# Performance work log

Measured on AMD Instinct MI355X. Metric: run time of the kernel, lower is better.

Reference implementation:

```python
import jax, jax.numpy as jnp
import numpy as np

K = 7  # kernel_size


def setup_inputs() -> dict:
    key = jax.random.key(0)
    k1, k2 = jax.random.split(key)
    kernels = jax.random.normal(k1, (4, K, K, 256, 256), dtype=jnp.float32)
    features = jax.random.normal(k2, (4, 96, 256, 256), dtype=jnp.float32)
    return {"kernels": kernels, "features": features}


def reference(kernels, features):
    # kernels: [b, k, k, h, w]; features: [b, c, h, w]
    # Equivalent to unfold(features) viewed as [b,c,k,k,h,w] contracted with
    # kernels via einsum 'bcklhw,bklhw->bchw', but computed as a fused sum of
    # k*k shifted products to avoid materializing the k^2-larger intermediate.
    b, c, h, w = features.shape
    k = kernels.shape[1]
    p = k // 2
    fpad = jnp.pad(features, ((0, 0), (0, 0), (p, p), (p, p)))
    out = jnp.zeros_like(features)
    for i in range(k):  # small fixed loop over kernel taps (k*k = 49)
        for j in range(k):
            out = out + fpad[:, :, i:i + h, j:j + w] * kernels[:, i, j][:, None]
    return out
```

## Files before the change

### kernel.cpp

```cpp
#include <hip/hip_runtime.h>
#include <hip/hip_bf16.h>


#define BATCH 4
#define CHAN 96
#define HW_ 256
#define HWPIX 65536
#define KS 7
#define XT 64
#define YT 16
#define NTHR 512
#define BT_K 24
#define BT_NROW (KS * BT_K)
#define BT_STRIP (16 * BT_NROW + 8)
#define BT_BUF (4 * BT_STRIP)
#define KVALS (KS * KS * XT)
#define KSPT 7
#define FTOT ((size_t)BATCH * CHAN * HWPIX)

typedef __attribute__((ext_vector_type(8))) short short8v;
typedef __attribute__((ext_vector_type(4))) float f32x4;

union S8 { short8v s; unsigned u[4]; };

static __device__ __forceinline__ unsigned pkbf(float a, float b) {
    union { __hip_bfloat162 h; unsigned u; } c;
    c.h = __float22bfloat162_rn(make_float2(a, b));
    return c.u;
}
static __device__ __forceinline__ short bfbits(float x) {
    union { __hip_bfloat16 h; short s; } c;
    c.h = __float2bfloat16(x);
    return c.s;
}

struct AF { float4 v[3][2]; };

__global__ __launch_bounds__(NTHR)
void svconv_mfma4(const float* __restrict__ K_, const float* __restrict__ F_,
                  float* __restrict__ O_) {
    __shared__ short BT[2 * BT_BUF];

    const int tid = threadIdx.x;
    const int xt = blockIdx.x, yt = blockIdx.y, b = blockIdx.z;
    const int gx0 = xt * XT, gy0 = yt * YT;
    const int wave = tid >> 6, lane = tid & 63;
    const int nt = wave & 3, ch = wave >> 2;
    const int n = lane & 15, kb = lane >> 4;

    const int xs = gx0 - 4 + nt * 16 + kb * 8;
    const float* lo = F_;
    const float* hiq = F_ + FTOT - 4;
    const float* abase[3];
#pragma unroll
    for (int ct = 0; ct < 3; ++ct)
        abase[ct] = F_ + ((size_t)(b * CHAN + ch * 48 + ct * 16 + n)) * HWPIX + xs;

    unsigned xm[4];
#pragma unroll
    for (int i = 0; i < 4; ++i) {
        unsigned m0 = ((unsigned)(xs + 2 * i) < (unsigned)HW_) ? 0xFFFFu : 0u;
        unsigned m1 = ((unsigned)(xs + 2 * i + 1) < (unsigned)HW_) ? 0xFFFFu : 0u;
        xm[i] = m0 | (m1 << 16);
    }

    short8v ar[8][3];

    auto issueA = [&](int yr, AF& f) {
#pragma unroll
        for (int ct = 0; ct < 3; ++ct) {
            const float* p = abase[ct] + (size_t)yr * HW_;
            const float* p0 = p;
            const float* p1 = p + 4;
            p0 = p0 < lo ? lo : (p0 > hiq ? hiq : p0);
            p1 = p1 < lo ? lo : (p1 > hiq ? hiq : p1);
            f.v[ct][0] = *(const float4*)p0;
            f.v[ct][1] = *(const float4*)p1;
        }
    };
    auto commitA = [&](int slot, const AF& f, bool yok) {
#pragma unroll
        for (int ct = 0; ct < 3; ++ct) {
            S8 v;
            if (yok) {
                v.u[0] = pkbf(f.v[ct][0].x, f.v[ct][0].y) & xm[0];
                v.u[1] = pkbf(f.v[ct][0].z, f.v[ct][0].w) & xm[1];
                v.u[2] = pkbf(f.v[ct][1].x, f.v[ct][1].y) & xm[2];
                v.u[3] = pkbf(f.v[ct][1].z, f.v[ct][1].w) & xm[3];
            } else {
                v.u[0] = 0; v.u[1] = 0; v.u[2] = 0; v.u[3] = 0;
            }
            ar[slot][ct] = v.s;
        }
    };

    int kgoff[KSPT], kldsoff[KSPT];
#pragma unroll
    for (int i = 0; i < KSPT; ++i) {
        int idx = tid + NTHR * i;
        if (idx < KVALS) {
            int dydx = idx >> 6, xl = idx & 63;
            int dy = dydx / KS, dx = dydx - KS * dy;
            int sn = xl & 15, snt = xl >> 4;
            kgoff[i] = dydx * HWPIX + gx0 + xl;
            kldsoff[i] = snt * BT_STRIP + sn * BT_NROW + dy * BT_K + (sn + dx + 1);
        } else { kgoff[i] = 0; kldsoff[i] = -1; }
    }
    const float* Kb = K_ + (size_t)b * KS * KS * HWPIX;

    {
        unsigned* bt32 = (unsigned*)BT;
#pragma unroll
        for (int i = 0; i < 22; ++i) {
            int idx = tid + NTHR * i;
            if (idx < BT_BUF) bt32[idx] = 0u;
        }
    }

    float kr0[KSPT];
#pragma unroll
    for (int i = 0; i < KSPT; ++i)
        kr0[i] = (kldsoff[i] >= 0) ? Kb[kgoff[i] + (size_t)gy0 * HW_] : 0.f;

    __syncthreads();

    AF afa, afb;
    issueA(gy0 - 3, afa);
#pragma unroll
    for (int r = 0; r < 7; ++r) {
        AF& cur = (r & 1) ? afb : afa;
        AF& nxt = (r & 1) ? afa : afb;
        if (r < 6) issueA(gy0 + r - 2, nxt);
        const int yr = gy0 + r - 3;
        commitA((r + 5) & 7, cur, (unsigned)yr < (unsigned)HW_);
    }

#pragma unroll
    for (int i = 0; i < KSPT; ++i)
        if (kldsoff[i] >= 0) BT[kldsoff[i]] = bfbits(kr0[i]);

    const short8v bzero = {0, 0, 0, 0, 0, 0, 0, 0};
    float* ob = O_ + ((size_t)(b * CHAN + ch * 48 + kb * 4)) * HWPIX
              + gx0 + nt * 16 + n;
    float krf[KSPT];
    AF af;

#pragma unroll
    for (int t = 0; t < YT; ++t) {
        const int y = gy0 + t;
        __syncthreads();

        if (t < YT - 1) {
#pragma unroll
            for (int i = 0; i < KSPT; ++i)
                krf[i] = (kldsoff[i] >= 0)
                       ? Kb[kgoff[i] + (size_t)(y + 1) * HW_] : 0.f;
        }
        const bool pyok = (y + 4 < HW_);
        if (pyok) issueA(y + 4, af);

        const short* btp = BT + (t & 1) * BT_BUF + nt * BT_STRIP + n * BT_NROW + kb * 8;
        short8v bfr[KS];
#pragma unroll
        for (int dy = 0; dy < KS; ++dy)
            bfr[dy] = (kb < 3) ? *(const short8v*)(btp + dy * BT_K) : bzero;

        f32x4 acc0 = {0,0,0,0}, acc1 = {0,0,0,0}, acc2 = {0,0,0,0};
#pragma unroll
        for (int dy = 0; dy < KS; ++dy) {
            const int sl = (t + dy + 5) & 7;
            acc0 = __builtin_amdgcn_mfma_f32_16x16x32_bf16(ar[sl][0], bfr[dy], acc0, 0, 0, 0);
            acc1 = __builtin_amdgcn_mfma_f32_16x16x32_bf16(ar[sl][1], bfr[dy], acc1, 0, 0, 0);
            acc2 = __builtin_amdgcn_mfma_f32_16x16x32_bf16(ar[sl][2], bfr[dy], acc2, 0, 0, 0);
        }

        {
            float* op = ob + (size_t)y * HW_;
#pragma unroll
            for (int r = 0; r < 4; ++r) {
                op[(size_t)r * HWPIX]        = acc0[r];
                op[(size_t)(16 + r) * HWPIX] = acc1[r];
                op[(size_t)(32 + r) * HWPIX] = acc2[r];
            }
        }

        commitA((t + 4) & 7, af, pyok);

        if (t < YT - 1) {
            short* btw = BT + ((t + 1) & 1) * BT_BUF;
#pragma unroll
            for (int i = 0; i < KSPT; ++i)
                if (kldsoff[i] >= 0) btw[kldsoff[i]] = bfbits(krf[i]);
        }
    }
}

extern "C" void kernel_launch(void* const* d_in, const int* in_sizes, int n_in,
                              void* d_out, int out_size, void* d_ws, size_t ws_size,
                              hipStream_t stream) {
    const float* kernels  = (const float*)d_in[0];
    const float* features = (const float*)d_in[1];
    float* out = (float*)d_out;

    dim3 grid(HW_ / XT, HW_ / YT, BATCH);
    dim3 block(NTHR);
    svconv_mfma4<<<grid, block, 0, stream>>>(kernels, features, out);
}
```

Baseline: 83.91 us.

## Shrink x-tile to 16 with one channel tile per wave and shift-register A rows

Narrows the block tile to 16 columns and uses 6 waves, each computing a single 16-channel tile, instead of 8 waves covering 3 channel tiles over 64 columns. This cuts per-thread registers (one A tile per row instead of three) and LDS per block, and adds a launch-bounds occupancy hint. The rolling A window becomes a register shift chain and the time loop is no longer unrolled. In exchange, each block reloads more halo columns and more kernel-weight staging relative to its output, and the grid is four times larger.

```diff
diff --git a/kernel.cpp b/kernel.cpp
--- a/kernel.cpp
+++ b/kernel.cpp
@@ -7,15 +7,13 @@
 #define HW_ 256
 #define HWPIX 65536
 #define KS 7
-#define XT 64
+#define XT 16
 #define YT 16
-#define NTHR 512
+#define NTHR 384
 #define BT_K 24
 #define BT_NROW (KS * BT_K)
-#define BT_STRIP (16 * BT_NROW + 8)
-#define BT_BUF (4 * BT_STRIP)
+#define BT_BUF (16 * BT_NROW)
 #define KVALS (KS * KS * XT)
-#define KSPT 7
 #define FTOT ((size_t)BATCH * CHAN * HWPIX)
 
 typedef __attribute__((ext_vector_type(8))) short short8v;
@@ -34,10 +32,8 @@
     return c.s;
 }
 
-struct AF { float4 v[3][2]; };
-
-__global__ __launch_bounds__(NTHR)
-void svconv_mfma4(const float* __restrict__ K_, const float* __restrict__ F_,
+__global__ __launch_bounds__(NTHR, 3)
+void svconv_mfma5(const float* __restrict__ K_, const float* __restrict__ F_,
                   float* __restrict__ O_) {
     __shared__ short BT[2 * BT_BUF];
 
@@ -45,152 +41,153 @@
     const int xt = blockIdx.x, yt = blockIdx.y, b = blockIdx.z;
     const int gx0 = xt * XT, gy0 = yt * YT;
     const int wave = tid >> 6, lane = tid & 63;
-    const int nt = wave & 3, ch = wave >> 2;
     const int n = lane & 15, kb = lane >> 4;
-
-    const int xs = gx0 - 4 + nt * 16 + kb * 8;
+    const int c0 = wave * 16;
+
+    const int kcl = (kb == 3) ? 0 : kb;
+    const int xs = gx0 - 4 + kcl * 8;
+    const float* abase = F_ + ((size_t)(b * CHAN + c0 + n)) * HWPIX + xs;
     const float* lo = F_;
     const float* hiq = F_ + FTOT - 4;
-    const float* abase[3];
+
+    unsigned xm0, xm1, xm2, xm3;
+    {
+        unsigned m[4];
 #pragma unroll
-    for (int ct = 0; ct < 3; ++ct)
-        abase[ct] = F_ + ((size_t)(b * CHAN + ch * 48 + ct * 16 + n)) * HWPIX + xs;
-
-    unsigned xm[4];
+        for (int i = 0; i < 4; ++i) {
+            unsigned a0 = ((unsigned)(xs + 2 * i) < (unsigned)HW_) ? 0xFFFFu : 0u;
+            unsigned a1 = ((unsigned)(xs + 2 * i + 1) < (unsigned)HW_) ? 0xFFFFu : 0u;
+            m[i] = a0 | (a1 << 16);
+        }
+        xm0 = m[0]; xm1 = m[1]; xm2 = m[2]; xm3 = m[3];
+    }
+
+#define AISSUE(F0, F1, yr) do {                                           \
+        const float* p = abase + (size_t)(yr) * HW_;                      \
+        const float* q0 = p;     q0 = q0 < lo ? lo : (q0 > hiq ? hiq : q0); \
+        const float* q1 = p + 4; q1 = q1 < lo ? lo : (q1 > hiq ? hiq : q1); \
+        F0 = *(const float4*)q0; F1 = *(const float4*)q1;                 \
+    } while (0)
+
+#define ACOMMIT(DST, F0, F1, YOK) do {                                    \
+        S8 v_;                                                            \
+        if (YOK) {                                                        \
+            v_.u[0] = pkbf(F0.x, F0.y) & xm0;                             \
+            v_.u[1] = pkbf(F0.z, F0.w) & xm1;                             \
+            v_.u[2] = pkbf(F1.x, F1.y) & xm2;                             \
+            v_.u[3] = pkbf(F1.z, F1.w) & xm3;                             \
+        } else { v_.u[0] = 0; v_.u[1] = 0; v_.u[2] = 0; v_.u[3] = 0; }    \
+        DST = v_.s;                                                       \
+    } while (0)
+
+    int kg0, kg1, kg2, kld0, kld1, kld2;
+    {
+        int kg[3], kld[3];
 #pragma unroll
-    for (int i = 0; i < 4; ++i) {
-        unsigned m0 = ((unsigned)(xs + 2 * i) < (unsigned)HW_) ? 0xFFFFu : 0u;
-        unsigned m1 = ((unsigned)(xs + 2 * i + 1) < (unsigned)HW_) ? 0xFFFFu : 0u;
-        xm[i] = m0 | (m1 << 16);
-    }
-
-    short8v ar[8][3];
-
-    auto issueA = [&](int yr, AF& f) {
-#pragma unroll
-        for (int ct = 0; ct < 3; ++ct) {
-            const float* p = abase[ct] + (size_t)yr * HW_;
-            const float* p0 = p;
-            const float* p1 = p + 4;
-            p0 = p0 < lo ? lo : (p0 > hiq ? hiq : p0);
-            p1 = p1 < lo ? lo : (p1 > hiq ? hiq : p1);
-            f.v[ct][0] = *(const float4*)p0;
-            f.v[ct][1] = *(const float4*)p1;
-        }
-    };
-    auto commitA = [&](int slot, const AF& f, bool yok) {
-#pragma unroll
-        for (int ct = 0; ct < 3; ++ct) {
-            S8 v;
-            if (yok) {
-                v.u[0] = pkbf(f.v[ct][0].x, f.v[ct][0].y) & xm[0];
-                v.u[1] = pkbf(f.v[ct][0].z, f.v[ct][0].w) & xm[1];
-                v.u[2] = pkbf(f.v[ct][1].x, f.v[ct][1].y) & xm[2];
-                v.u[3] = pkbf(f.v[ct][1].z, f.v[ct][1].w) & xm[3];
-            } else {
-                v.u[0] = 0; v.u[1] = 0; v.u[2] = 0; v.u[3] = 0;
-            }
-            ar[slot][ct] = v.s;
-        }
-    };
-
-    int kgoff[KSPT], kldsoff[KSPT];
-#pragma unroll
-    for (int i = 0; i < KSPT; ++i) {
-        int idx = tid + NTHR * i;
-        if (idx < KVALS) {
-            int dydx = idx >> 6, xl = idx & 63;
-            int dy = dydx / KS, dx = dydx - KS * dy;
-            int sn = xl & 15, snt = xl >> 4;
-            kgoff[i] = dydx * HWPIX + gx0 + xl;
-            kldsoff[i] = snt * BT_STRIP + sn * BT_NROW + dy * BT_K + (sn + dx + 1);
-        } else { kgoff[i] = 0; kldsoff[i] = -1; }
+        for (int i = 0; i < 3; ++i) {
+            int idx = tid + NTHR * i;
+            if (idx < KVALS) {
+                int dydx = idx >> 4, xl = idx & 15;
+                int dy = dydx / KS, dx = dydx - KS * dy;
+                kg[i] = dydx * HWPIX + gx0 + xl;
+                kld[i] = xl * BT_NROW + dy * BT_K + (xl + dx + 1);
+            } else { kg[i] = 0; kld[i] = -1; }
+        }
+        kg0 = kg[0]; kg1 = kg[1]; kg2 = kg[2];
+        kld0 = kld[0]; kld1 = kld[1]; kld2 = kld[2];
     }
     const float* Kb = K_ + (size_t)b * KS * KS * HWPIX;
 
     {
         unsigned* bt32 = (unsigned*)BT;
 #pragma unroll
-        for (int i = 0; i < 22; ++i) {
-            int idx = tid + NTHR * i;
-            if (idx < BT_BUF) bt32[idx] = 0u;
-        }
-    }
-
-    float kr0[KSPT];
-#pragma unroll
-    for (int i = 0; i < KSPT; ++i)
-        kr0[i] = (kldsoff[i] >= 0) ? Kb[kgoff[i] + (size_t)gy0 * HW_] : 0.f;
+        for (int i = 0; i < 7; ++i) bt32[tid + NTHR * i] = 0u;
+    }
+
+    float krA = (kld0 >= 0) ? Kb[kg0 + (size_t)gy0 * HW_] : 0.f;
+    float krB = (kld1 >= 0) ? Kb[kg1 + (size_t)gy0 * HW_] : 0.f;
+    float krC = (kld2 >= 0) ? Kb[kg2 + (size_t)gy0 * HW_] : 0.f;
+
+    float4 fa0, fa1, fb0, fb1, fc0, fc1, fd0, fd1, fe0, fe1, ff0, ff1, fg0, fg1;
+    AISSUE(fa0, fa1, gy0 - 3); AISSUE(fb0, fb1, gy0 - 2);
+    AISSUE(fc0, fc1, gy0 - 1); AISSUE(fd0, fd1, gy0);
+    AISSUE(fe0, fe1, gy0 + 1); AISSUE(ff0, ff1, gy0 + 2);
+    AISSUE(fg0, fg1, gy0 + 3);
 
     __syncthreads();
 
-    AF afa, afb;
-    issueA(gy0 - 3, afa);
-#pragma unroll
-    for (int r = 0; r < 7; ++r) {
-        AF& cur = (r & 1) ? afb : afa;
-        AF& nxt = (r & 1) ? afa : afb;
-        if (r < 6) issueA(gy0 + r - 2, nxt);
-        const int yr = gy0 + r - 3;
-        commitA((r + 5) & 7, cur, (unsigned)yr < (unsigned)HW_);
-    }
-
-#pragma unroll
-    for (int i = 0; i < KSPT; ++i)
-        if (kldsoff[i] >= 0) BT[kldsoff[i]] = bfbits(kr0[i]);
+    short8v s0, s1, s2, s3, s4, s5, s6;
+    ACOMMIT(s0, fa0, fa1, gy0 - 3 >= 0);
+    ACOMMIT(s1, fb0, fb1, gy0 - 2 >= 0);
+    ACOMMIT(s2, fc0, fc1, gy0 - 1 >= 0);
+    ACOMMIT(s3, fd0, fd1, true);
+    ACOMMIT(s4, fe0, fe1, true);
+    ACOMMIT(s5, ff0, ff1, true);
+    ACOMMIT(s6, fg0, fg1, true);
+
+    if (kld0 >= 0) BT[kld0] = bfbits(krA);
+    if (kld1 >= 0) BT[kld1] = bfbits(krB);
+    if (kld2 >= 0) BT[kld2] = bfbits(krC);
 
     const short8v bzero = {0, 0, 0, 0, 0, 0, 0, 0};
-    float* ob = O_ + ((size_t)(b * CHAN + ch * 48 + kb * 4)) * HWPIX
-              + gx0 + nt * 16 + n;
-    float krf[KSPT];
-    AF af;
-
-#pragma unroll
+    float* ob = O_ + ((size_t)(b * CHAN + c0 + kb * 4)) * HWPIX + gx0 + n;
+    const int kb8 = kb * 8;
+
     for (int t = 0; t < YT; ++t) {
         const int y = gy0 + t;
         __syncthreads();
 
+        float kA = 0.f, kB = 0.f, kC = 0.f;
         if (t < YT - 1) {
-#pragma unroll
-            for (int i = 0; i < KSPT; ++i)
-                krf[i] = (kldsoff[i] >= 0)
-                       ? Kb[kgoff[i] + (size_t)(y + 1) * HW_] : 0.f;
+            const size_t yo = (size_t)(y + 1) * HW_;
+            if (kld0 >= 0) kA = Kb[kg0 + yo];
+            if (kld1 >= 0) kB = Kb[kg1 + yo];
+            if (kld2 >= 0) kC = Kb[kg2 + yo];
         }
         const bool pyok = (y + 4 < HW_);
-        if (pyok) issueA(y + 4, af);
-
-        const short* btp = BT + (t & 1) * BT_BUF + nt * BT_STRIP + n * BT_NROW + kb * 8;
-        short8v bfr[KS];
-#pragma unroll
-        for (int dy = 0; dy < KS; ++dy)
-            bfr[dy] = (kb < 3) ? *(const short8v*)(btp + dy * BT_K) : bzero;
-
-        f32x4 acc0 = {0,0,0,0}, acc1 = {0,0,0,0}, acc2 = {0,0,0,0};
-#pragma unroll
-        for (int dy = 0; dy < KS; ++dy) {
-            const int sl = (t + dy + 5) & 7;
-            acc0 = __builtin_amdgcn_mfma_f32_16x16x32_bf16(ar[sl][0], bfr[dy], acc0, 0, 0, 0);
-            acc1 = __builtin_amdgcn_mfma_f32_16x16x32_bf16(ar[sl][1], bfr[dy], acc1, 0, 0, 0);
-            acc2 = __builtin_amdgcn_mfma_f32_16x16x32_bf16(ar[sl][2], bfr[dy], acc2, 0, 0, 0);
-        }
+        float4 g0, g1;
+        AISSUE(g0, g1, y + 4);
+
+        const short* btp = BT + (t & 1) * BT_BUF + n * BT_NROW + kb8;
+        short8v b0, b1, b2, b3, b4, b5, b6;
+        if (kb < 3) {
+            b0 = *(const short8v*)(btp);
+            b1 = *(const short8v*)(btp + 1 * BT_K);
+            b2 = *(const short8v*)(btp + 2 * BT_K);
+            b3 = *(const short8v*)(btp + 3 * BT_K);
+            b4 = *(const short8v*)(btp + 4 * BT_K);
+            b5 = *(const short8v*)(btp + 5 * BT_K);
+            b6 = *(const short8v*)(btp + 6 * BT_K);
+        } else {
+            b0 = bzero; b1 = bzero; b2 = bzero; b3 = bzero;
+            b4 = bzero; b5 = bzero; b6 = bzero;
+        }
+
+        f32x4 acc = {0.f, 0.f, 0.f, 0.f};
+        acc = __builtin_amdgcn_mfma_f32_16x16x32_bf16(s0, b0, acc, 0, 0, 0);
+        acc = __builtin_amdgcn_mfma_f32_16x16x32_bf16(s1, b1, acc, 0, 0, 0);
+        acc = __builtin_amdgcn_mfma_f32_16x16x32_bf16(s2, b2, acc, 0, 0, 0);
+        acc = __builtin_amdgcn_mfma_f32_16x16x32_bf16(s3, b3, acc, 0, 0, 0);
+        acc = __builtin_amdgcn_mfma_f32_16x16x32_bf16(s4, b4, acc, 0, 0, 0);
+        acc = __builtin_amdgcn_mfma_f32_16x16x32_bf16(s5, b5, acc, 0, 0, 0);
+        acc = __builtin_amdgcn_mfma_f32_16x16x32_bf16(s6, b6, acc, 0, 0, 0);
 
         {
             float* op = ob + (size_t)y * HW_;
-#pragma unroll
-            for (int r = 0; r < 4; ++r) {
-                op[(size_t)r * HWPIX]        = acc0[r];
-                op[(size_t)(16 + r) * HWPIX] = acc1[r];
-                op[(size_t)(32 + r) * HWPIX] = acc2[r];
-            }
-        }
-
-        commitA((t + 4) & 7, af, pyok);
+            op[0]                    = acc[0];
+            op[(size_t)1 * HWPIX]    = acc[1];
+            op[(size_t)2 * HWPIX]    = acc[2];
+            op[(size_t)3 * HWPIX]    = acc[3];
+        }
+
+        s0 = s1; s1 = s2; s2 = s3; s3 = s4; s4 = s5; s5 = s6;
+        ACOMMIT(s6, g0, g1, pyok);
 
         if (t < YT - 1) {
             short* btw = BT + ((t + 1) & 1) * BT_BUF;
-#pragma unroll
-            for (int i = 0; i < KSPT; ++i)
-                if (kldsoff[i] >= 0) btw[kldsoff[i]] = bfbits(krf[i]);
+            if (kld0 >= 0) btw[kld0] = bfbits(kA);
+            if (kld1 >= 0) btw[kld1] = bfbits(kB);
+            if (kld2 >= 0) btw[kld2] = bfbits(kC);
         }
     }
 }
@@ -204,5 +201,5 @@
 
     dim3 grid(HW_ / XT, HW_ / YT, BATCH);
     dim3 block(NTHR);
-    svconv_mfma4<<<grid, block, 0, stream>>>(kernels, features, out);
-}
+    svconv_mfma5<<<grid, block, 0, stream>>>(kernels, features, out);
+}
```

After: 112.4 us. 34.0% more time.

## Stage feature rows in an LDS ring buffer shared across waves instead of registers

Applied to the files above, without the earlier changes.

Feature rows are no longer held in per-lane register arrays with redundant halo loads. They are now loaded cooperatively into a shared-memory ring of eight bf16 rows, and MFMA A operands are read from LDS. The tile shrinks to 32 columns with 256 threads, and the weight buffer becomes single-buffered with two barriers per row. This is meant to cut register pressure and duplicate global traffic so occupancy can rise, at the cost of extra LDS reads, more barriers and dynamic LDS use.

```diff
diff --git a/kernel.cpp b/kernel.cpp
--- a/kernel.cpp
+++ b/kernel.cpp
@@ -7,21 +7,25 @@
 #define HW_ 256
 #define HWPIX 65536
 #define KS 7
-#define XT 64
+#define XT 32
 #define YT 16
-#define NTHR 512
+#define NTHR 256
+#define XPITCH 40
+#define ROWSTRIDE (CHAN * XPITCH)
+#define RING_S (8 * ROWSTRIDE)
+#define NXP 20
+#define RSLOTS (CHAN * NXP)
+#define RSPT 8
 #define BT_K 24
 #define BT_NROW (KS * BT_K)
-#define BT_STRIP (16 * BT_NROW + 8)
-#define BT_BUF (4 * BT_STRIP)
+#define BT_STRIP (16 * BT_NROW)
+#define BT_S (2 * BT_STRIP)
 #define KVALS (KS * KS * XT)
 #define KSPT 7
-#define FTOT ((size_t)BATCH * CHAN * HWPIX)
+#define LDS_BYTES ((RING_S + BT_S) * 2)
 
 typedef __attribute__((ext_vector_type(8))) short short8v;
 typedef __attribute__((ext_vector_type(4))) float f32x4;
-
-union S8 { short8v s; unsigned u[4]; };
 
 static __device__ __forceinline__ unsigned pkbf(float a, float b) {
     union { __hip_bfloat162 h; unsigned u; } c;
@@ -34,144 +38,136 @@
     return c.s;
 }
 
-struct AF { float4 v[3][2]; };
+#define LDS_BARRIER() asm volatile("s_waitcnt lgkmcnt(0)\ns_barrier" ::: "memory")
 
 __global__ __launch_bounds__(NTHR)
-void svconv_mfma4(const float* __restrict__ K_, const float* __restrict__ F_,
-                  float* __restrict__ O_) {
-    __shared__ short BT[2 * BT_BUF];
+void svconv_v12(const float* __restrict__ K_, const float* __restrict__ F_,
+                float* __restrict__ O_) {
+    extern __shared__ short lds[];
+    unsigned* ring32 = (unsigned*)lds;
+    short* BT = lds + RING_S;
 
     const int tid = threadIdx.x;
     const int xt = blockIdx.x, yt = blockIdx.y, b = blockIdx.z;
     const int gx0 = xt * XT, gy0 = yt * YT;
     const int wave = tid >> 6, lane = tid & 63;
-    const int nt = wave & 3, ch = wave >> 2;
+    const int nt = wave & 1, ch = wave >> 1;
     const int n = lane & 15, kb = lane >> 4;
 
-    const int xs = gx0 - 4 + nt * 16 + kb * 8;
-    const float* lo = F_;
-    const float* hiq = F_ + FTOT - 4;
-    const float* abase[3];
-#pragma unroll
-    for (int ct = 0; ct < 3; ++ct)
-        abase[ct] = F_ + ((size_t)(b * CHAN + ch * 48 + ct * 16 + n)) * HWPIX + xs;
-
-    unsigned xm[4];
-#pragma unroll
-    for (int i = 0; i < 4; ++i) {
-        unsigned m0 = ((unsigned)(xs + 2 * i) < (unsigned)HW_) ? 0xFFFFu : 0u;
-        unsigned m1 = ((unsigned)(xs + 2 * i + 1) < (unsigned)HW_) ? 0xFFFFu : 0u;
-        xm[i] = m0 | (m1 << 16);
-    }
-
-    short8v ar[8][3];
-
-    auto issueA = [&](int yr, AF& f) {
-#pragma unroll
-        for (int ct = 0; ct < 3; ++ct) {
-            const float* p = abase[ct] + (size_t)yr * HW_;
-            const float* p0 = p;
-            const float* p1 = p + 4;
-            p0 = p0 < lo ? lo : (p0 > hiq ? hiq : p0);
-            p1 = p1 < lo ? lo : (p1 > hiq ? hiq : p1);
-            f.v[ct][0] = *(const float4*)p0;
-            f.v[ct][1] = *(const float4*)p1;
-        }
-    };
-    auto commitA = [&](int slot, const AF& f, bool yok) {
-#pragma unroll
-        for (int ct = 0; ct < 3; ++ct) {
-            S8 v;
-            if (yok) {
-                v.u[0] = pkbf(f.v[ct][0].x, f.v[ct][0].y) & xm[0];
-                v.u[1] = pkbf(f.v[ct][0].z, f.v[ct][0].w) & xm[1];
-                v.u[2] = pkbf(f.v[ct][1].x, f.v[ct][1].y) & xm[2];
-                v.u[3] = pkbf(f.v[ct][1].z, f.v[ct][1].w) & xm[3];
-            } else {
-                v.u[0] = 0; v.u[1] = 0; v.u[2] = 0; v.u[3] = 0;
-            }
-            ar[slot][ct] = v.s;
-        }
-    };
-
-    int kgoff[KSPT], kldsoff[KSPT];
+    int rgo[RSPT]; unsigned rls[RSPT]; unsigned rm[RSPT]; bool rv[RSPT];
+#pragma unroll
+    for (int k = 0; k < RSPT; ++k) {
+        const int idx = tid + NTHR * k;
+        const bool valid = idx < RSLOTS;
+        const int c = valid ? idx / NXP : 0;
+        const int xi = valid ? idx - c * NXP : 0;
+        const int fx0 = gx0 - 4 + 2 * xi;
+        const int fxc = fx0 < 0 ? 0 : (fx0 > HW_ - 2 ? HW_ - 2 : fx0);
+        rgo[k] = c * HWPIX + fxc;
+        rls[k] = (unsigned)(c * NXP + xi);
+        unsigned m0 = ((unsigned)fx0 < (unsigned)HW_) ? 0xFFFFu : 0u;
+        unsigned m1 = ((unsigned)(fx0 + 1) < (unsigned)HW_) ? 0xFFFF0000u : 0u;
+        rm[k] = m0 | m1;
+        rv[k] = valid;
+    }
+    const float* Fb = F_ + (size_t)b * CHAN * HWPIX;
+
+    int kg[KSPT], kl[KSPT];
 #pragma unroll
     for (int i = 0; i < KSPT; ++i) {
-        int idx = tid + NTHR * i;
+        const int idx = tid + NTHR * i;
         if (idx < KVALS) {
-            int dydx = idx >> 6, xl = idx & 63;
-            int dy = dydx / KS, dx = dydx - KS * dy;
-            int sn = xl & 15, snt = xl >> 4;
-            kgoff[i] = dydx * HWPIX + gx0 + xl;
-            kldsoff[i] = snt * BT_STRIP + sn * BT_NROW + dy * BT_K + (sn + dx + 1);
-        } else { kgoff[i] = 0; kldsoff[i] = -1; }
+            const int dydx = idx >> 5, xl = idx & 31;
+            const int dy = dydx / KS, dx = dydx - KS * dy;
+            const int sn = xl & 15, snt = xl >> 4;
+            kg[i] = dydx * HWPIX + gx0 + xl;
+            kl[i] = snt * BT_STRIP + sn * BT_NROW + dy * BT_K + (sn + dx + 1);
+        } else { kg[i] = 0; kl[i] = -1; }
     }
     const float* Kb = K_ + (size_t)b * KS * KS * HWPIX;
 
     {
         unsigned* bt32 = (unsigned*)BT;
 #pragma unroll
-        for (int i = 0; i < 22; ++i) {
-            int idx = tid + NTHR * i;
-            if (idx < BT_BUF) bt32[idx] = 0u;
-        }
-    }
-
-    float kr0[KSPT];
+        for (int i = 0; i < 11; ++i) {
+            const int idx = tid + NTHR * i;
+            if (idx < BT_S / 2) bt32[idx] = 0u;
+        }
+    }
+
+    for (int r = -3; r <= 3; ++r) {
+        const int yr = gy0 + r;
+        const bool yok = (unsigned)yr < (unsigned)HW_;
+        const int yrc = yr < 0 ? 0 : (yr > HW_ - 1 ? HW_ - 1 : yr);
+        const unsigned sbase = (unsigned)((yr & 7) * RSLOTS);
+        float2 v[RSPT];
+#pragma unroll
+        for (int k = 0; k < RSPT; ++k)
+            v[k] = *(const float2*)(Fb + rgo[k] + (size_t)yrc * HW_);
+#pragma unroll
+        for (int k = 0; k < RSPT; ++k) {
+            unsigned w = pkbf(v[k].x, v[k].y) & rm[k];
+            if (!yok) w = 0u;
+            if (rv[k]) ring32[sbase + rls[k]] = w;
+        }
+    }
+
+    LDS_BARRIER();
+
+    {
+        float kr0[KSPT];
+#pragma unroll
+        for (int i = 0; i < KSPT; ++i)
+            kr0[i] = (kl[i] >= 0) ? Kb[kg[i] + (size_t)gy0 * HW_] : 0.f;
+#pragma unroll
+        for (int i = 0; i < KSPT; ++i)
+            if (kl[i] >= 0) BT[kl[i]] = bfbits(kr0[i]);
+    }
+
+    float2 rr[RSPT];
+    float kr[KSPT];
+#pragma unroll
+    for (int k = 0; k < RSPT; ++k)
+        rr[k] = *(const float2*)(Fb + rgo[k] + (size_t)(gy0 + 4) * HW_);
 #pragma unroll
     for (int i = 0; i < KSPT; ++i)
-        kr0[i] = (kldsoff[i] >= 0) ? Kb[kgoff[i] + (size_t)gy0 * HW_] : 0.f;
-
-    __syncthreads();
-
-    AF afa, afb;
-    issueA(gy0 - 3, afa);
-#pragma unroll
-    for (int r = 0; r < 7; ++r) {
-        AF& cur = (r & 1) ? afb : afa;
-        AF& nxt = (r & 1) ? afa : afb;
-        if (r < 6) issueA(gy0 + r - 2, nxt);
-        const int yr = gy0 + r - 3;
-        commitA((r + 5) & 7, cur, (unsigned)yr < (unsigned)HW_);
-    }
-
-#pragma unroll
-    for (int i = 0; i < KSPT; ++i)
-        if (kldsoff[i] >= 0) BT[kldsoff[i]] = bfbits(kr0[i]);
-
-    const short8v bzero = {0, 0, 0, 0, 0, 0, 0, 0};
+        kr[i] = (kl[i] >= 0) ? Kb[kg[i] + (size_t)(gy0 + 1) * HW_] : 0.f;
+
+    const int kcl8 = (kb == 3) ? 0 : kb * 8;
+    const short* btp = BT + nt * BT_STRIP + n * BT_NROW + kb * 8;
+    const int arow = (ch * 48 + n) * XPITCH + nt * 16 + kcl8;
     float* ob = O_ + ((size_t)(b * CHAN + ch * 48 + kb * 4)) * HWPIX
               + gx0 + nt * 16 + n;
-    float krf[KSPT];
-    AF af;
-
-#pragma unroll
+    const short8v bzero = {0, 0, 0, 0, 0, 0, 0, 0};
+
+#pragma unroll 1
     for (int t = 0; t < YT; ++t) {
         const int y = gy0 + t;
-        __syncthreads();
-
-        if (t < YT - 1) {
-#pragma unroll
-            for (int i = 0; i < KSPT; ++i)
-                krf[i] = (kldsoff[i] >= 0)
-                       ? Kb[kgoff[i] + (size_t)(y + 1) * HW_] : 0.f;
-        }
-        const bool pyok = (y + 4 < HW_);
-        if (pyok) issueA(y + 4, af);
-
-        const short* btp = BT + (t & 1) * BT_BUF + nt * BT_STRIP + n * BT_NROW + kb * 8;
-        short8v bfr[KS];
-#pragma unroll
-        for (int dy = 0; dy < KS; ++dy)
-            bfr[dy] = (kb < 3) ? *(const short8v*)(btp + dy * BT_K) : bzero;
+        LDS_BARRIER();
+
+        short8v b0, b1, b2, b3, b4, b5, b6;
+        if (kb < 3) {
+            b0 = *(const short8v*)(btp);
+            b1 = *(const short8v*)(btp + 1 * BT_K);
+            b2 = *(const short8v*)(btp + 2 * BT_K);
+            b3 = *(const short8v*)(btp + 3 * BT_K);
+            b4 = *(const short8v*)(btp + 4 * BT_K);
+            b5 = *(const short8v*)(btp + 5 * BT_K);
+            b6 = *(const short8v*)(btp + 6 * BT_K);
+        } else {
+            b0 = bzero; b1 = bzero; b2 = bzero; b3 = bzero;
+            b4 = bzero; b5 = bzero; b6 = bzero;
+        }
 
         f32x4 acc0 = {0,0,0,0}, acc1 = {0,0,0,0}, acc2 = {0,0,0,0};
 #pragma unroll
         for (int dy = 0; dy < KS; ++dy) {
-            const int sl = (t + dy + 5) & 7;
-            acc0 = __builtin_amdgcn_mfma_f32_16x16x32_bf16(ar[sl][0], bfr[dy], acc0, 0, 0, 0);
-            acc1 = __builtin_amdgcn_mfma_f32_16x16x32_bf16(ar[sl][1], bfr[dy], acc1, 0, 0, 0);
-            acc2 = __builtin_amdgcn_mfma_f32_16x16x32_bf16(ar[sl][2], bfr[dy], acc2, 0, 0, 0);
+            const short8v bf = dy == 0 ? b0 : dy == 1 ? b1 : dy == 2 ? b2 :
+                               dy == 3 ? b3 : dy == 4 ? b4 : dy == 5 ? b5 : b6;
+            const short* ap = lds + ((y + dy + 5) & 7) * ROWSTRIDE + arow;
+            acc0 = __builtin_amdgcn_mfma_f32_16x16x32_bf16(*(const short8v*)(ap), bf, acc0, 0, 0, 0);
+            acc1 = __builtin_amdgcn_mfma_f32_16x16x32_bf16(*(const short8v*)(ap + 16 * XPITCH), bf, acc1, 0, 0, 0);
+            acc2 = __builtin_amdgcn_mfma_f32_16x16x32_bf16(*(const short8v*)(ap + 32 * XPITCH), bf, acc2, 0, 0, 0);
         }
 
         {
@@ -184,13 +180,31 @@
             }
         }
 
-        commitA((t + 4) & 7, af, pyok);
+        LDS_BARRIER();
 
         if (t < YT - 1) {
-            short* btw = BT + ((t + 1) & 1) * BT_BUF;
+            const bool yok = (y + 4) < HW_;
+            const unsigned sbase = (unsigned)(((y + 4) & 7) * RSLOTS);
+#pragma unroll
+            for (int k = 0; k < RSPT; ++k) {
+                unsigned w = pkbf(rr[k].x, rr[k].y) & rm[k];
+                if (!yok) w = 0u;
+                if (rv[k]) ring32[sbase + rls[k]] = w;
+            }
 #pragma unroll
             for (int i = 0; i < KSPT; ++i)
-                if (kldsoff[i] >= 0) btw[kldsoff[i]] = bfbits(krf[i]);
+                if (kl[i] >= 0) BT[kl[i]] = bfbits(kr[i]);
+        }
+
+        if (t < YT - 2) {
+            const int yr = y + 5;
+            const int yrc = yr > HW_ - 1 ? HW_ - 1 : yr;
+#pragma unroll
+            for (int k = 0; k < RSPT; ++k)
+                rr[k] = *(const float2*)(Fb + rgo[k] + (size_t)yrc * HW_);
+#pragma unroll
+            for (int i = 0; i < KSPT; ++i)
+                kr[i] = (kl[i] >= 0) ? Kb[kg[i] + (size_t)(y + 2) * HW_] : 0.f;
         }
     }
 }
@@ -202,7 +216,10 @@
     const float* features = (const float*)d_in[1];
     float* out = (float*)d_out;
 
+    hipFuncSetAttribute(reinterpret_cast<const void*>(&svconv_v12),
+                        hipFuncAttributeMaxDynamicSharedMemorySize, LDS_BYTES);
+
     dim3 grid(HW_ / XT, HW_ / YT, BATCH);
     dim3 block(NTHR);
-    svconv_mfma4<<<grid, block, 0, stream>>>(kernels, features, out);
-}
+    svconv_v12<<<grid, block, LDS_BYTES, stream>>>(kernels, features, out);
+}
```

New measurement: 84.11 us. About the same (+0.2%).
